# Performance work log

Measured on AMD Instinct MI355X. Metric: run time of the kernel, lower is better.

## Reference

```python
import jax, jax.numpy as jnp
import numpy as np

B, S, HID = 1, 2048, 2048
H, D = 16, 128          # num heads, head_dim (H*D == HID)
L = 32                  # compression / selection block size
NB = S // L             # number of key blocks
NSEL = 8                # top-n selected blocks per query
WIN = 512               # sliding window size
SCALE = 1.0 / np.sqrt(D)
NEG = -1e9


def rotate_half(x):
    x1, x2 = x[..., : x.shape[-1] // 2], x[..., x.shape[-1] // 2 :]
    return jnp.concatenate([-x2, x1], axis=-1)


def rope_tables(dim, end, theta=10000.0):
    freqs = 1.0 / theta ** (jnp.arange(0, dim, 2, dtype=jnp.float32) / dim)
    ang = jnp.outer(jnp.arange(end, dtype=jnp.float32), freqs)  # [end, dim/2]
    cos = jnp.concatenate([jnp.cos(ang), jnp.cos(ang)], axis=-1)  # [end, dim]
    sin = jnp.concatenate([jnp.sin(ang), jnp.sin(ang)], axis=-1)
    return cos, sin


def setup_inputs() -> dict:
    key = jax.random.key(0)
    ks = jax.random.split(key, 10)
    std = 0.02
    return {
        "hidden_states": jax.random.normal(ks[0], (B, S, HID), jnp.float32),
        "Wq": jax.random.normal(ks[1], (HID, H * D), jnp.float32) * std,
        "bq": jnp.zeros((H * D,), jnp.float32),
        "Wk": jax.random.normal(ks[2], (HID, H * D), jnp.float32) * std,
        "bk": jnp.zeros((H * D,), jnp.float32),
        "Wv": jax.random.normal(ks[3], (HID, H * D), jnp.float32) * std,
        "bv": jnp.zeros((H * D,), jnp.float32),
        "Wg": jax.random.normal(ks[4], (H, D, 3), jnp.float32) * std,
        "bg": jnp.zeros((3,), jnp.float32),
    }


def _nsa_forward(hidden_states, Wq, bq, Wk, bk, Wv, bv, Wg, bg):
    # projections -> [B, H, S, D]
    def proj(W, b):
        return (hidden_states @ W + b).reshape(B, S, H, D).transpose(0, 2, 1, 3)

    q, k, v = proj(Wq, bq), proj(Wk, bk), proj(Wv, bv)

    cos, sin = rope_tables(D, S)  # [S, D]
    cos, sin = cos[None, None], sin[None, None]
    q = q * cos + rotate_half(q) * sin
    k = k * cos + rotate_half(k) * sin

    i = jnp.arange(S)
    t = jnp.arange(S)
    causal = t[None, :] <= i[:, None]  # [S, S]

    # ---- compressed branch: block mean-pooled K/V ----
    k_cmp = k.reshape(B, H, NB, L, D).mean(axis=3)  # [B,H,NB,D]
    v_cmp = v.reshape(B, H, NB, L, D).mean(axis=3)
    # block j visible if it ends at or before query position i
    blk_ok = ((jnp.arange(NB) + 1) * L - 1)[None, :] <= i[:, None]  # [S, NB]
    s_cmp = jnp.einsum("bhid,bhjd->bhij", q, k_cmp) * SCALE  # [B,H,S,NB]
    p_cmp = jax.nn.softmax(jnp.where(blk_ok[None, None], s_cmp, NEG), axis=-1)
    has_blk = blk_ok.any(axis=-1).astype(q.dtype)[None, None, :, None]  # [1,1,S,1]
    out_cmp = jnp.einsum("bhij,bhjd->bhid", p_cmp, v_cmp) * has_blk

    # ---- selection branch: top-n blocks from compressed scores ----
    idx = jax.lax.top_k(p_cmp, NSEL)[1]  # [B,H,S,NSEL]
    block_sel = (idx[..., None] == jnp.arange(NB)).any(axis=-2)  # [B,H,S,NB]
    cur_blk = (i[:, None] // L) == jnp.arange(NB)[None, :]  # always include own block
    block_sel = block_sel | cur_blk[None, None]
    tok_sel = jnp.take(block_sel, t // L, axis=-1)  # [B,H,S,S]
    mask_sel = tok_sel & causal[None, None]

    s = jnp.einsum("bhid,bhjd->bhij", q, k) * SCALE
    p_sel = jax.nn.softmax(jnp.where(mask_sel, s, NEG), axis=-1)
    out_sel = jnp.einsum("bhij,bhjd->bhid", p_sel, v)

    # ---- sliding-window branch ----
    mask_win = causal & ((i[:, None] - t[None, :]) < WIN)
    p_win = jax.nn.softmax(jnp.where(mask_win[None, None], s, NEG), axis=-1)
    out_win = jnp.einsum("bhij,bhjd->bhid", p_win, v)

    # ---- gated combine ----
    g = jax.nn.sigmoid(jnp.einsum("bhsd,hdg->bhsg", q, Wg) + bg)  # [B,H,S,3]
    out = (g[..., 0:1] * out_cmp + g[..., 1:2] * out_sel + g[..., 2:3] * out_win)
    return out.transpose(0, 2, 1, 3).reshape(B, S, H * D)


def reference(hidden_states, Wq, bq, Wk, bk, Wv, bv, Wg, bg):
    return _nsa_forward(hidden_states, Wq, bq, Wk, bk, Wv, bv, Wg, bg)
```

## Files before the change

### kernel.cpp

```cpp
#include <hip/hip_runtime.h>


#define SCALE_F 0.08838834764831845f
#define SCL2E   (0.08838834764831845f * 1.4426950408889634f)

typedef short  bf16x8 __attribute__((ext_vector_type(8)));
typedef short  s16x4  __attribute__((ext_vector_type(4)));
typedef float  f32x4  __attribute__((ext_vector_type(4)));

__device__ __forceinline__ unsigned short f2bfu(float x){
    unsigned u = __builtin_bit_cast(unsigned, x);
    u = (u + 0x7FFFu + ((u >> 16) & 1u)) >> 16;
    return (unsigned short)u;
}
__device__ __forceinline__ float bf2f(unsigned short b){
    unsigned u = ((unsigned)b) << 16;
    return __builtin_bit_cast(float, u);
}
__device__ __forceinline__ f32x4 mfma16(bf16x8 a, bf16x8 b, f32x4 c){
    return __builtin_amdgcn_mfma_f32_16x16x32_bf16(a, b, c, 0, 0, 0);
}

__global__ __launch_bounds__(64) void rope_table_k(float* __restrict__ ct,
                                                   float* __restrict__ st){
    int s = blockIdx.x, j = threadIdx.x;
    float fr  = 1.0f / powf(10000.0f, (float)j * (1.0f / 64.0f));
    float ang = (float)s * fr;
    ct[s * 64 + j] = cosf(ang);
    st[s * 64 + j] = sinf(ang);
}

template <bool LO>
__global__ __launch_bounds__(256) void prep_split(const float* __restrict__ src,
                                                  unsigned short* __restrict__ hi,
                                                  unsigned short* __restrict__ lo){
    size_t i = ((size_t)blockIdx.x * 256 + threadIdx.x) * 4;
    float4 x = *(const float4*)&src[i];
    unsigned short h0 = f2bfu(x.x), h1 = f2bfu(x.y), h2 = f2bfu(x.z), h3 = f2bfu(x.w);
    s16x4 hv; hv[0] = (short)h0; hv[1] = (short)h1; hv[2] = (short)h2; hv[3] = (short)h3;
    *(s16x4*)&hi[i] = hv;
    if (LO){
        s16x4 lv;
        lv[0] = (short)f2bfu(x.x - bf2f(h0)); lv[1] = (short)f2bfu(x.y - bf2f(h1));
        lv[2] = (short)f2bfu(x.z - bf2f(h2)); lv[3] = (short)f2bfu(x.w - bf2f(h3));
        *(s16x4*)&lo[i] = lv;
    }
}

__global__ __launch_bounds__(256) void prep_wT(const float* __restrict__ W,
                                               unsigned short* __restrict__ Th,
                                               unsigned short* __restrict__ Tl){
    __shared__ float T[64][65];
    const int k0 = blockIdx.x * 64, n0 = blockIdx.y * 64;
    const int tid = (int)threadIdx.x;
    #pragma unroll
    for (int it = 0; it < 16; ++it){
        int idx = tid + it * 256;
        int r = idx >> 6, c = idx & 63;
        T[c][r] = W[(size_t)(k0 + r) * 2048 + n0 + c];
    }
    __syncthreads();
    #pragma unroll
    for (int it = 0; it < 16; ++it){
        int idx = tid + it * 256;
        int n = idx >> 6, k = idx & 63;
        float v = T[n][k];
        unsigned short h = f2bfu(v);
        Th[(size_t)(n0 + n) * 2048 + k0 + k] = h;
        if (Tl) Tl[(size_t)(n0 + n) * 2048 + k0 + k] = f2bfu(v - bf2f(h));
    }
}

template <int P>
__global__ __launch_bounds__(256) void gemm_bf(
    const unsigned short* __restrict__ Ah, const unsigned short* __restrict__ Al,
    const unsigned short* __restrict__ Bh, const unsigned short* __restrict__ Bl,
    const float* __restrict__ bias,
    float* __restrict__ outF, unsigned short* __restrict__ outT)
{
    const unsigned short* Ap[2] = {Ah, Al};
    const unsigned short* Bp[2] = {Bh, Bl};
    const int m0  = blockIdx.x * 128;
    const int h   = blockIdx.y;
    const int tid = (int)threadIdx.x;
    const int l   = tid & 63, w = tid >> 6;
    const int wr  = w >> 1,  wc = w & 1;
    const int cc  = l & 15,  g  = l >> 4;

    __shared__ short As[P][128][40];
    __shared__ short Bs[P][128][40];

    f32x4 acc[4][4] = {};
    bf16x8 ra[P][2], rb[P][2];

    auto LOADSTEP = [&](int k0){
        #pragma unroll
        for (int p = 0; p < P; ++p)
            #pragma unroll
            for (int it = 0; it < 2; ++it){
                int c = tid + it * 256;
                int row = c >> 2, col8 = (c & 3) * 8;
                ra[p][it] = *(const bf16x8*)&Ap[p][(size_t)(m0 + row) * 2048 + k0 + col8];
                rb[p][it] = *(const bf16x8*)&Bp[p][(size_t)(h * 128 + row) * 2048 + k0 + col8];
            }
    };
    auto STORESTEP = [&](){
        #pragma unroll
        for (int p = 0; p < P; ++p)
            #pragma unroll
            for (int it = 0; it < 2; ++it){
                int c = tid + it * 256;
                int row = c >> 2, col8 = (c & 3) * 8;
                *(bf16x8*)&As[p][row][col8] = ra[p][it];
                *(bf16x8*)&Bs[p][row][col8] = rb[p][it];
            }
    };

    LOADSTEP(0); STORESTEP(); __syncthreads();
    for (int k0 = 0; k0 < 2048; k0 += 32){
        bool more = (k0 + 32) < 2048;
        if (more) LOADSTEP(k0 + 32);

        bf16x8 ah[4], bh[4];
        #pragma unroll
        for (int mt = 0; mt < 4; ++mt)
            ah[mt] = *(const bf16x8*)&As[0][wr * 64 + mt * 16 + cc][g * 8];
        #pragma unroll
        for (int nt = 0; nt < 4; ++nt)
            bh[nt] = *(const bf16x8*)&Bs[0][wc * 64 + nt * 16 + cc][g * 8];
        if (P == 2){
            bf16x8 al[4], bl[4];
            #pragma unroll
            for (int mt = 0; mt < 4; ++mt)
                al[mt] = *(const bf16x8*)&As[P - 1][wr * 64 + mt * 16 + cc][g * 8];
            #pragma unroll
            for (int nt = 0; nt < 4; ++nt)
                bl[nt] = *(const bf16x8*)&Bs[P - 1][wc * 64 + nt * 16 + cc][g * 8];
            #pragma unroll
            for (int mt = 0; mt < 4; ++mt)
                #pragma unroll
                for (int nt = 0; nt < 4; ++nt){
                    acc[mt][nt] = mfma16(ah[mt], bh[nt], acc[mt][nt]);
                    acc[mt][nt] = mfma16(ah[mt], bl[nt], acc[mt][nt]);
                    acc[mt][nt] = mfma16(al[mt], bh[nt], acc[mt][nt]);
                }
        } else {
            #pragma unroll
            for (int mt = 0; mt < 4; ++mt)
                #pragma unroll
                for (int nt = 0; nt < 4; ++nt)
                    acc[mt][nt] = mfma16(ah[mt], bh[nt], acc[mt][nt]);
        }
        __syncthreads();
        if (more){ STORESTEP(); __syncthreads(); }
    }

    #pragma unroll
    for (int mt = 0; mt < 4; ++mt)
        #pragma unroll
        for (int nt = 0; nt < 4; ++nt)
            #pragma unroll
            for (int j = 0; j < 4; ++j){
                int srow = m0 + wr * 64 + mt * 16 + g * 4 + j;
                int col  = wc * 64 + nt * 16 + cc;
                float v = acc[mt][nt][j] + bias[h * 128 + col];
                if (outF) outF[((size_t)h * 2048 + srow) * 128 + col] = v;
                else      outT[((size_t)h * 128 + col) * 2048 + srow] = f2bfu(v);
            }
}

__global__ __launch_bounds__(256) void rope_apply(
    float* __restrict__ qf, float* __restrict__ kf,
    const float* __restrict__ ct, const float* __restrict__ st)
{
    int idx = blockIdx.x * 256 + (int)threadIdx.x;
    int j = idx & 63;
    int s = (idx >> 6) & 2047;
    int h = (idx >> 17) & 15;
    int a = idx >> 21;
    float* p = (a ? kf : qf) + ((size_t)h * 2048 + s) * 128;
    float c = ct[s * 64 + j], sn = st[s * 64 + j];
    float x1 = p[j], x2 = p[j + 64];
    p[j]      = x1 * c - x2 * sn;
    p[j + 64] = x2 * c + x1 * sn;
}

__global__ __launch_bounds__(256) void cmp_mean(
    const float* __restrict__ kf, const unsigned short* __restrict__ vtbf,
    float* __restrict__ kcmp, float* __restrict__ vcmp)
{
    int idx = blockIdx.x * 256 + (int)threadIdx.x;
    int d  = idx & 127;
    int nb = (idx >> 7) & 63;
    int h  = idx >> 13;
    const float* kp = &kf[((size_t)h * 2048 + nb * 32) * 128 + d];
    float sk = 0.f;
    #pragma unroll
    for (int t = 0; t < 32; ++t) sk += kp[t * 128];
    const unsigned short* vp = &vtbf[((size_t)h * 128 + d) * 2048 + nb * 32];
    float sv = 0.f;
    #pragma unroll
    for (int t = 0; t < 32; ++t) sv += bf2f(vp[t]);
    kcmp[((size_t)h * 64 + nb) * 128 + d] = sk * 0.03125f;
    vcmp[((size_t)h * 64 + nb) * 128 + d] = sv * 0.03125f;
}

__global__ __launch_bounds__(256) void gates_k(
    const float* __restrict__ qf, const float* __restrict__ Wg,
    const float* __restrict__ bg, float* __restrict__ gout)
{
    int Gn = blockIdx.x * 256 + (int)threadIdx.x;
    int sub = Gn & 3, qh = Gn >> 2;
    if (sub == 3) return;
    int h = qh >> 11;
    const float* q  = &qf[(size_t)qh * 128];
    const float* wg = &Wg[(size_t)h * 384 + sub];
    float acc = 0.f;
    #pragma unroll 4
    for (int k = 0; k < 128; ++k) acc += q[k] * wg[k * 3];
    gout[(size_t)qh * 3 + sub] = 1.f / (1.f + expf(-(acc + bg[sub])));
}

__global__ __launch_bounds__(256) void cmp_attn(
    const float* __restrict__ qf, const float* __restrict__ kcmp,
    const float* __restrict__ vcmp, const float* __restrict__ gout,
    float* __restrict__ out, unsigned long long* __restrict__ bmask)
{
    const int h = blockIdx.y, qt = blockIdx.x, i0 = qt * 64;
    const int tid = (int)threadIdx.x;
    const int l = tid & 63, w = tid >> 6;
    const int ty = tid >> 4, tx = tid & 15;
    const int cc = l & 15, g = l >> 4;

    __shared__ __align__(16) char smem[65536];
    float4* qs4 = (float4*)smem;
    float4* kc4 = (float4*)(smem + 32768);
    unsigned short* vcT = (unsigned short*)smem;
    float* sc = (float*)(smem + 32768);
    unsigned short* ps = (unsigned short*)(smem + 32768 + 17408);

    #pragma unroll
    for (int it = 0; it < 8; ++it){
        int idx = tid + it * 256;
        int row = idx >> 5, c = idx & 31;
        int cs = c ^ ((row >> 2) & 7);
        qs4[row * 32 + cs] = *(const float4*)&qf[((size_t)h * 2048 + i0 + row) * 128 + c * 4];
        kc4[row * 32 + cs] = *(const float4*)&kcmp[((size_t)h * 64 + row) * 128 + c * 4];
    }
    __syncthreads();

    float acc[4][4] = {};
    #pragma unroll 2
    for (int k0 = 0; k0 < 32; ++k0){
        float4 qv[4], kv[4];
        #pragma unroll
        for (int j = 0; j < 4; ++j) qv[j] = qs4[(4 * ty + j) * 32 + (k0 ^ (ty & 7))];
        #pragma unroll
        for (int c = 0; c < 4; ++c) kv[c] = kc4[(4 * tx + c) * 32 + (k0 ^ (tx & 7))];
        #pragma unroll
        for (int j = 0; j < 4; ++j)
            #pragma unroll
            for (int c = 0; c < 4; ++c)
                acc[j][c] += qv[j].x * kv[c].x + qv[j].y * kv[c].y
                           + qv[j].z * kv[c].z + qv[j].w * kv[c].w;
    }
    __syncthreads();

    #pragma unroll
    for (int j = 0; j < 4; ++j){
        int r = 4 * ty + j, i = i0 + r;
        float4 sv;
        float* svp = (float*)&sv;
        #pragma unroll
        for (int c = 0; c < 4; ++c){
            int b = 4 * tx + c;
            svp[c] = (b * 32 + 31 <= i) ? acc[j][c] * SCALE_F : -1e9f;
        }
        *(float4*)&sc[r * 68 + 4 * tx] = sv;
    }
    #pragma unroll
    for (int it = 0; it < 8; ++it){
        int idx = tid + it * 256;
        int jb = idx >> 5, d4 = (idx & 31) * 4;
        float4 vx = *(const float4*)&vcmp[((size_t)h * 64 + jb) * 128 + d4];
        const float* vp = (const float*)&vx;
        #pragma unroll
        for (int jj = 0; jj < 4; ++jj)
            vcT[(d4 + jj) * 72 + jb] = f2bfu(vp[jj]);
    }
    __syncthreads();

    for (int qq = 0; qq < 16; ++qq){
        const int q = w * 16 + qq;
        float s = sc[q * 68 + l];
        float mx = s;
        #pragma unroll
        for (int off = 1; off < 64; off <<= 1) mx = fmaxf(mx, __shfl_xor(mx, off));
        float p = expf(s - mx);
        float sum = p;
        #pragma unroll
        for (int off = 1; off < 64; off <<= 1) sum += __shfl_xor(sum, off);
        p /= sum;
        ps[q * 72 + l] = f2bfu(p);

        unsigned long long sel = 1ULL << ((i0 + q) >> 5);
        unsigned long long key = (1ULL << 45) |
            ((unsigned long long)__builtin_bit_cast(unsigned, p) << 7) |
            (unsigned long long)(63 - l);
        #pragma unroll
        for (int it = 0; it < 8; ++it){
            unsigned long long k2 = key;
            #pragma unroll
            for (int off = 1; off < 64; off <<= 1){
                unsigned long long o = __shfl_xor(k2, off);
                k2 = (o > k2) ? o : k2;
            }
            int wb = 63 - (int)(k2 & 63ULL);
            sel |= 1ULL << wb;
            if (l == wb) key = 0ULL;
        }
        if (l == 0) bmask[(size_t)h * 2048 + i0 + q] = sel;
    }
    __syncthreads();

    f32x4 oacc[8] = {};
    #pragma unroll
    for (int kk = 0; kk < 2; ++kk){
        bf16x8 pa = *(const bf16x8*)&ps[(w * 16 + cc) * 72 + kk * 32 + g * 8];
        #pragma unroll
        for (int nt2 = 0; nt2 < 8; ++nt2){
            bf16x8 vfr = *(const bf16x8*)&vcT[(nt2 * 16 + cc) * 72 + kk * 32 + g * 8];
            oacc[nt2] = mfma16(pa, vfr, oacc[nt2]);
        }
    }
    #pragma unroll
    for (int j = 0; j < 4; ++j){
        int q = w * 16 + g * 4 + j, iq = i0 + q;
        float g0 = gout[((size_t)h * 2048 + iq) * 3];
        float f = (iq >= 31) ? g0 : 0.f;
        #pragma unroll
        for (int nt2 = 0; nt2 < 8; ++nt2)
            out[(size_t)iq * 2048 + h * 128 + nt2 * 16 + cc] = f * oacc[nt2][j];
    }
}

template <bool IS_SEL>
__global__ __launch_bounds__(256) void attn_main(
    const unsigned short* __restrict__ qbf,
    const unsigned short* __restrict__ kbf,
    const unsigned short* __restrict__ vtbf,
    const float* __restrict__ gates,
    const unsigned long long* __restrict__ bmask,
    float* __restrict__ out)
{
    const int h  = blockIdx.y;
    const int qt = IS_SEL ? 31 - (int)blockIdx.x : (int)blockIdx.x;
    const int i0 = qt * 64;
    const int tid = (int)threadIdx.x;
    const int l = tid & 63, w = tid >> 6;
    const int cc = l & 15,  g = l >> 4;

    __shared__ short Ks[64][136];
    __shared__ short Vt[128][72];
    __shared__ short Ps[4][16][72];

    unsigned long long um = 0;
    if (IS_SEL){
        um = bmask[(size_t)h * 2048 + i0 + l];
        #pragma unroll
        for (int off = 1; off < 64; off <<= 1) um |= __shfl_xor(um, off);
    }

    unsigned long long bm[4];
    int mrow[4];
    #pragma unroll
    for (int j = 0; j < 4; ++j){
        mrow[j] = i0 + w * 16 + g * 4 + j;
        bm[j] = IS_SEL ? bmask[(size_t)h * 2048 + mrow[j]] : 0ULL;
    }

    bf16x8 qfrag[4];
    {
        const unsigned short* qrow = &qbf[((size_t)h * 2048 + i0 + w * 16 + cc) * 128];
        #pragma unroll
        for (int kk = 0; kk < 4; ++kk)
            qfrag[kk] = *(const bf16x8*)&qrow[kk * 32 + g * 8];
    }

    f32x4 oacc[8] = {};
    float mrun[4], lrun[4];
    #pragma unroll
    for (int j = 0; j < 4; ++j){ mrun[j] = -1e30f; lrun[j] = 0.f; }

    const int chlo = IS_SEL ? 0 : (qt > 8 ? qt - 8 : 0);
    auto needed = [&](int ch)->bool {
        return IS_SEL ? (((um >> (2 * ch)) & 3ULL) != 0ULL) : true;
    };

    bf16x8 rk[4], rv[4];
    auto LOADC = [&](int ch){
        #pragma unroll
        for (int it = 0; it < 4; ++it){
            int c = tid + it * 256;
            rk[it] = *(const bf16x8*)&kbf[((size_t)h * 2048 + ch * 64 + (c >> 4)) * 128 + (c & 15) * 8];
            rv[it] = *(const bf16x8*)&vtbf[((size_t)h * 128 + (c >> 3)) * 2048 + ch * 64 + (c & 7) * 8];
        }
    };
    auto STOREC = [&](){
        #pragma unroll
        for (int it = 0; it < 4; ++it){
            int c = tid + it * 256;
            *(bf16x8*)&Ks[c >> 4][(c & 15) * 8] = rk[it];
            *(bf16x8*)&Vt[c >> 3][(c & 7) * 8] = rv[it];
        }
    };

    int cur = chlo;
    while (cur <= qt && !needed(cur)) ++cur;
    LOADC(cur); STOREC(); __syncthreads();

    while (cur <= qt){
        int nxt = cur + 1;
        while (nxt <= qt && !needed(nxt)) ++nxt;
        const bool more = (nxt <= qt);
        if (more) LOADC(nxt);

        f32x4 sacc[4] = {};
        #pragma unroll
        for (int kk = 0; kk < 4; ++kk)
            #pragma unroll
            for (int nt = 0; nt < 4; ++nt){
                bf16x8 kfr = *(const bf16x8*)&Ks[nt * 16 + cc][kk * 32 + g * 8];
                sacc[nt] = mfma16(qfrag[kk], kfr, sacc[nt]);
            }

        const int tbase = cur * 64;
        #pragma unroll
        for (int j = 0; j < 4; ++j){
            const int iq = mrow[j];
            float sj[4]; bool ok[4];
            float mx = -1e30f;
            #pragma unroll
            for (int nt = 0; nt < 4; ++nt){
                int t = tbase + nt * 16 + cc;
                bool o = (t <= iq) &&
                         (IS_SEL ? (((bm[j] >> (t >> 5)) & 1ULL) != 0ULL)
                                 : ((iq - t) < 512));
                float s = sacc[nt][j] * SCL2E;
                sj[nt] = s; ok[nt] = o;
                if (o) mx = fmaxf(mx, s);
            }
            #pragma unroll
            for (int off = 1; off < 16; off <<= 1)
                mx = fmaxf(mx, __shfl_xor(mx, off));
            float mnew = fmaxf(mrun[j], mx);
            float alpha = exp2f(mrun[j] - mnew);
            float psum = 0.f;
            #pragma unroll
            for (int nt = 0; nt < 4; ++nt){
                float p = ok[nt] ? exp2f(sj[nt] - mnew) : 0.f;
                psum += p;
                Ps[w][g * 4 + j][nt * 16 + cc] = (short)f2bfu(p);
            }
            #pragma unroll
            for (int off = 1; off < 16; off <<= 1)
                psum += __shfl_xor(psum, off);
            mrun[j] = mnew;
            lrun[j] = lrun[j] * alpha + psum;
            #pragma unroll
            for (int nt2 = 0; nt2 < 8; ++nt2) oacc[nt2][j] *= alpha;
        }
        __syncthreads();

        #pragma unroll
        for (int kk = 0; kk < 2; ++kk){
            bf16x8 pa = *(const bf16x8*)&Ps[w][cc][kk * 32 + g * 8];
            #pragma unroll
            for (int nt2 = 0; nt2 < 8; ++nt2){
                bf16x8 vfr = *(const bf16x8*)&Vt[nt2 * 16 + cc][kk * 32 + g * 8];
                oacc[nt2] = mfma16(pa, vfr, oacc[nt2]);
            }
        }
        __syncthreads();
        if (more){ STOREC(); __syncthreads(); }
        cur = more ? nxt : qt + 1;
    }

    const int GI = IS_SEL ? 1 : 2;
    #pragma unroll
    for (int j = 0; j < 4; ++j){
        const int iq = mrow[j];
        float gv  = gates[((size_t)h * 2048 + iq) * 3 + GI];
        float inv = gv / lrun[j];
        #pragma unroll
        for (int nt2 = 0; nt2 < 8; ++nt2){
            int d = nt2 * 16 + cc;
            out[(size_t)iq * 2048 + h * 128 + d] += oacc[nt2][j] * inv;
        }
    }
}

#define MB ((size_t)1 << 20)
#define OFF_QF   ((size_t)0)
#define OFF_KF   (16 * MB)
#define OFF_VT   (32 * MB)
#define OFF_XH   (40 * MB)
#define OFF_XL   (48 * MB)
#define OFF_WTH  (56 * MB)
#define OFF_WTL  (64 * MB)
#define OFF_COS  (72 * MB)
#define OFF_SIN  (72 * MB + 524288)
#define OFF_KC   (72 * MB + 1048576)
#define OFF_VC   (72 * MB + 1572864)
#define OFF_GATE (72 * MB + 2097152)
#define OFF_BM   (72 * MB + 2490368)

extern "C" void kernel_launch(void* const* d_in, const int* in_sizes, int n_in,
                              void* d_out, int out_size, void* d_ws, size_t ws_size,
                              hipStream_t stream)
{
    const float* X  = (const float*)d_in[0];
    const float* Wq = (const float*)d_in[1];
    const float* bq = (const float*)d_in[2];
    const float* Wk = (const float*)d_in[3];
    const float* bk = (const float*)d_in[4];
    const float* Wv = (const float*)d_in[5];
    const float* bv = (const float*)d_in[6];
    const float* Wg = (const float*)d_in[7];
    const float* bg = (const float*)d_in[8];
    float* out = (float*)d_out;

    char* ws = (char*)d_ws;
    float* qf   = (float*)(ws + OFF_QF);
    float* kf   = (float*)(ws + OFF_KF);
    unsigned short* vtbf = (unsigned short*)(ws + OFF_VT);
    unsigned short* Xh   = (unsigned short*)(ws + OFF_XH);
    unsigned short* Xl   = (unsigned short*)(ws + OFF_XL);
    unsigned short* WTh  = (unsigned short*)(ws + OFF_WTH);
    unsigned short* WTl  = (unsigned short*)(ws + OFF_WTL);
    unsigned short* qbf  = (unsigned short*)(ws + OFF_XH);
    unsigned short* kbf  = (unsigned short*)(ws + OFF_XL);
    float* cost  = (float*)(ws + OFF_COS);
    float* sint  = (float*)(ws + OFF_SIN);
    float* kcmp  = (float*)(ws + OFF_KC);
    float* vcmp  = (float*)(ws + OFF_VC);
    float* gatesb = (float*)(ws + OFF_GATE);
    unsigned long long* bmaskb = (unsigned long long*)(ws + OFF_BM);

    rope_table_k<<<2048, 64, 0, stream>>>(cost, sint);
    prep_split<true><<<4096, 256, 0, stream>>>(X, Xh, Xl);

    prep_wT<<<dim3(32, 32), 256, 0, stream>>>(Wq, WTh, WTl);
    gemm_bf<2><<<dim3(16, 16), 256, 0, stream>>>(Xh, Xl, WTh, WTl, bq, qf, nullptr);
    prep_wT<<<dim3(32, 32), 256, 0, stream>>>(Wk, WTh, WTl);
    gemm_bf<2><<<dim3(16, 16), 256, 0, stream>>>(Xh, Xl, WTh, WTl, bk, kf, nullptr);
    prep_wT<<<dim3(32, 32), 256, 0, stream>>>(Wv, WTh, nullptr);
    gemm_bf<1><<<dim3(16, 16), 256, 0, stream>>>(Xh, nullptr, WTh, nullptr, bv, nullptr, vtbf);

    rope_apply<<<16384, 256, 0, stream>>>(qf, kf, cost, sint);
    prep_split<false><<<4096, 256, 0, stream>>>(qf, qbf, nullptr);
    prep_split<false><<<4096, 256, 0, stream>>>(kf, kbf, nullptr);

    cmp_mean<<<512, 256, 0, stream>>>(kf, vtbf, kcmp, vcmp);
    gates_k<<<512, 256, 0, stream>>>(qf, Wg, bg, gatesb);
    cmp_attn<<<dim3(32, 16), 256, 0, stream>>>(qf, kcmp, vcmp, gatesb, out, bmaskb);

    attn_main<false><<<dim3(32, 16), 256, 0, stream>>>(qbf, kbf, vtbf, gatesb, bmaskb, out);
    attn_main<true><<<dim3(32, 16), 256, 0, stream>>>(qbf, kbf, vtbf, gatesb, bmaskb, out);
}
```

Measured before the change: 597.7 us.

## Batch QKV projections, fuse gates and bf16 conversion, merge attention branches

Merges the three weight transposes and three projection GEMMs into single z-indexed launches when the workspace is large enough. RoPE now writes bf16 copies directly, so two conversion passes are dropped. The gate computation moves into the compressed-attention kernel. The selected and sliding-window attention kernels become one launch with atomic output accumulation, XOR-swizzled shared memory and a lazy-rescale online softmax. These changes cut launch count, memory passes and bank conflicts. In exchange they add atomics, a workspace-size dependence and the possibility of a different floating-point summation order.

```diff
diff --git a/kernel.cpp b/kernel.cpp
--- a/kernel.cpp
+++ b/kernel.cpp
@@ -30,7 +30,6 @@
     st[s * 64 + j] = sinf(ang);
 }
 
-template <bool LO>
 __global__ __launch_bounds__(256) void prep_split(const float* __restrict__ src,
                                                   unsigned short* __restrict__ hi,
                                                   unsigned short* __restrict__ lo){
@@ -39,17 +38,24 @@
     unsigned short h0 = f2bfu(x.x), h1 = f2bfu(x.y), h2 = f2bfu(x.z), h3 = f2bfu(x.w);
     s16x4 hv; hv[0] = (short)h0; hv[1] = (short)h1; hv[2] = (short)h2; hv[3] = (short)h3;
     *(s16x4*)&hi[i] = hv;
-    if (LO){
-        s16x4 lv;
-        lv[0] = (short)f2bfu(x.x - bf2f(h0)); lv[1] = (short)f2bfu(x.y - bf2f(h1));
-        lv[2] = (short)f2bfu(x.z - bf2f(h2)); lv[3] = (short)f2bfu(x.w - bf2f(h3));
-        *(s16x4*)&lo[i] = lv;
-    }
-}
-
-__global__ __launch_bounds__(256) void prep_wT(const float* __restrict__ W,
-                                               unsigned short* __restrict__ Th,
-                                               unsigned short* __restrict__ Tl){
+    s16x4 lv;
+    lv[0] = (short)f2bfu(x.x - bf2f(h0)); lv[1] = (short)f2bfu(x.y - bf2f(h1));
+    lv[2] = (short)f2bfu(x.z - bf2f(h2)); lv[3] = (short)f2bfu(x.w - bf2f(h3));
+    *(s16x4*)&lo[i] = lv;
+}
+
+__global__ __launch_bounds__(256) void prep_wT3(
+    const float* __restrict__ W0, const float* __restrict__ W1,
+    const float* __restrict__ W2,
+    unsigned short* __restrict__ Th0, unsigned short* __restrict__ Tl0,
+    unsigned short* __restrict__ Th1, unsigned short* __restrict__ Tl1,
+    unsigned short* __restrict__ Th2)
+{
+    const int z = blockIdx.z;
+    const float* W = (z == 0) ? W0 : (z == 1) ? W1 : W2;
+    unsigned short* Th = (z == 0) ? Th0 : (z == 1) ? Th1 : Th2;
+    unsigned short* Tl = (z == 0) ? Tl0 : (z == 1) ? Tl1 : nullptr;
+
     __shared__ float T[64][65];
     const int k0 = blockIdx.x * 64, n0 = blockIdx.y * 64;
     const int tid = (int)threadIdx.x;
@@ -71,15 +77,22 @@
     }
 }
 
-template <int P>
-__global__ __launch_bounds__(256) void gemm_bf(
-    const unsigned short* __restrict__ Ah, const unsigned short* __restrict__ Al,
-    const unsigned short* __restrict__ Bh, const unsigned short* __restrict__ Bl,
-    const float* __restrict__ bias,
-    float* __restrict__ outF, unsigned short* __restrict__ outT)
+__global__ __launch_bounds__(256, 3) void gemm3(
+    const unsigned short* __restrict__ Xh, const unsigned short* __restrict__ Xl,
+    const unsigned short* __restrict__ Bqh, const unsigned short* __restrict__ Bql,
+    const unsigned short* __restrict__ Bkh, const unsigned short* __restrict__ Bkl,
+    const unsigned short* __restrict__ Bvh,
+    const float* __restrict__ bq, const float* __restrict__ bk,
+    const float* __restrict__ bv,
+    float* __restrict__ qf, float* __restrict__ kf,
+    unsigned short* __restrict__ vtbf, int zbase)
 {
-    const unsigned short* Ap[2] = {Ah, Al};
-    const unsigned short* Bp[2] = {Bh, Bl};
+    const int z = zbase + (int)blockIdx.z;
+    const bool split = (z < 2);
+    const unsigned short* Bh = (z == 0) ? Bqh : (z == 1) ? Bkh : Bvh;
+    const unsigned short* Bl = (z == 0) ? Bql : Bkl;
+    const float* bias        = (z == 0) ? bq  : (z == 1) ? bk  : bv;
+
     const int m0  = blockIdx.x * 128;
     const int h   = blockIdx.y;
     const int tid = (int)threadIdx.x;
@@ -87,33 +100,37 @@
     const int wr  = w >> 1,  wc = w & 1;
     const int cc  = l & 15,  g  = l >> 4;
 
-    __shared__ short As[P][128][40];
-    __shared__ short Bs[P][128][40];
+    __shared__ short As[2][128][40];
+    __shared__ short Bs[2][128][40];
 
     f32x4 acc[4][4] = {};
-    bf16x8 ra[P][2], rb[P][2];
+    bf16x8 rah[2], ral[2], rbh[2], rbl[2];
 
     auto LOADSTEP = [&](int k0){
         #pragma unroll
-        for (int p = 0; p < P; ++p)
-            #pragma unroll
-            for (int it = 0; it < 2; ++it){
-                int c = tid + it * 256;
-                int row = c >> 2, col8 = (c & 3) * 8;
-                ra[p][it] = *(const bf16x8*)&Ap[p][(size_t)(m0 + row) * 2048 + k0 + col8];
-                rb[p][it] = *(const bf16x8*)&Bp[p][(size_t)(h * 128 + row) * 2048 + k0 + col8];
-            }
+        for (int it = 0; it < 2; ++it){
+            int c = tid + it * 256;
+            int row = c >> 2, col8 = (c & 3) * 8;
+            rah[it] = *(const bf16x8*)&Xh[(size_t)(m0 + row) * 2048 + k0 + col8];
+            rbh[it] = *(const bf16x8*)&Bh[(size_t)(h * 128 + row) * 2048 + k0 + col8];
+            if (split){
+                ral[it] = *(const bf16x8*)&Xl[(size_t)(m0 + row) * 2048 + k0 + col8];
+                rbl[it] = *(const bf16x8*)&Bl[(size_t)(h * 128 + row) * 2048 + k0 + col8];
+            }
+        }
     };
     auto STORESTEP = [&](){
         #pragma unroll
-        for (int p = 0; p < P; ++p)
-            #pragma unroll
-            for (int it = 0; it < 2; ++it){
-                int c = tid + it * 256;
-                int row = c >> 2, col8 = (c & 3) * 8;
-                *(bf16x8*)&As[p][row][col8] = ra[p][it];
-                *(bf16x8*)&Bs[p][row][col8] = rb[p][it];
-            }
+        for (int it = 0; it < 2; ++it){
+            int c = tid + it * 256;
+            int row = c >> 2, col8 = (c & 3) * 8;
+            *(bf16x8*)&As[0][row][col8] = rah[it];
+            *(bf16x8*)&Bs[0][row][col8] = rbh[it];
+            if (split){
+                *(bf16x8*)&As[1][row][col8] = ral[it];
+                *(bf16x8*)&Bs[1][row][col8] = rbl[it];
+            }
+        }
     };
 
     LOADSTEP(0); STORESTEP(); __syncthreads();
@@ -128,14 +145,14 @@
         #pragma unroll
         for (int nt = 0; nt < 4; ++nt)
             bh[nt] = *(const bf16x8*)&Bs[0][wc * 64 + nt * 16 + cc][g * 8];
-        if (P == 2){
+        if (split){
             bf16x8 al[4], bl[4];
             #pragma unroll
             for (int mt = 0; mt < 4; ++mt)
-                al[mt] = *(const bf16x8*)&As[P - 1][wr * 64 + mt * 16 + cc][g * 8];
+                al[mt] = *(const bf16x8*)&As[1][wr * 64 + mt * 16 + cc][g * 8];
             #pragma unroll
             for (int nt = 0; nt < 4; ++nt)
-                bl[nt] = *(const bf16x8*)&Bs[P - 1][wc * 64 + nt * 16 + cc][g * 8];
+                bl[nt] = *(const bf16x8*)&Bs[1][wc * 64 + nt * 16 + cc][g * 8];
             #pragma unroll
             for (int mt = 0; mt < 4; ++mt)
                 #pragma unroll
@@ -164,13 +181,15 @@
                 int srow = m0 + wr * 64 + mt * 16 + g * 4 + j;
                 int col  = wc * 64 + nt * 16 + cc;
                 float v = acc[mt][nt][j] + bias[h * 128 + col];
-                if (outF) outF[((size_t)h * 2048 + srow) * 128 + col] = v;
-                else      outT[((size_t)h * 128 + col) * 2048 + srow] = f2bfu(v);
+                if (z == 0)      qf[((size_t)h * 2048 + srow) * 128 + col] = v;
+                else if (z == 1) kf[((size_t)h * 2048 + srow) * 128 + col] = v;
+                else             vtbf[((size_t)h * 128 + col) * 2048 + srow] = f2bfu(v);
             }
 }
 
 __global__ __launch_bounds__(256) void rope_apply(
     float* __restrict__ qf, float* __restrict__ kf,
+    unsigned short* __restrict__ qbb, unsigned short* __restrict__ kbb,
     const float* __restrict__ ct, const float* __restrict__ st)
 {
     int idx = blockIdx.x * 256 + (int)threadIdx.x;
@@ -178,11 +197,15 @@
     int s = (idx >> 6) & 2047;
     int h = (idx >> 17) & 15;
     int a = idx >> 21;
-    float* p = (a ? kf : qf) + ((size_t)h * 2048 + s) * 128;
+    size_t off = ((size_t)h * 2048 + s) * 128;
+    float* p = (a ? kf : qf) + off;
+    unsigned short* pb = (a ? kbb : qbb) + off;
     float c = ct[s * 64 + j], sn = st[s * 64 + j];
     float x1 = p[j], x2 = p[j + 64];
-    p[j]      = x1 * c - x2 * sn;
-    p[j + 64] = x2 * c + x1 * sn;
+    float y1 = x1 * c - x2 * sn;
+    float y2 = x2 * c + x1 * sn;
+    p[j]      = y1;  p[j + 64]  = y2;
+    pb[j] = f2bfu(y1); pb[j + 64] = f2bfu(y2);
 }
 
 __global__ __launch_bounds__(256) void cmp_mean(
@@ -205,26 +228,12 @@
     vcmp[((size_t)h * 64 + nb) * 128 + d] = sv * 0.03125f;
 }
 
-__global__ __launch_bounds__(256) void gates_k(
-    const float* __restrict__ qf, const float* __restrict__ Wg,
-    const float* __restrict__ bg, float* __restrict__ gout)
-{
-    int Gn = blockIdx.x * 256 + (int)threadIdx.x;
-    int sub = Gn & 3, qh = Gn >> 2;
-    if (sub == 3) return;
-    int h = qh >> 11;
-    const float* q  = &qf[(size_t)qh * 128];
-    const float* wg = &Wg[(size_t)h * 384 + sub];
-    float acc = 0.f;
-    #pragma unroll 4
-    for (int k = 0; k < 128; ++k) acc += q[k] * wg[k * 3];
-    gout[(size_t)qh * 3 + sub] = 1.f / (1.f + expf(-(acc + bg[sub])));
-}
-
 __global__ __launch_bounds__(256) void cmp_attn(
     const float* __restrict__ qf, const float* __restrict__ kcmp,
-    const float* __restrict__ vcmp, const float* __restrict__ gout,
-    float* __restrict__ out, unsigned long long* __restrict__ bmask)
+    const float* __restrict__ vcmp,
+    const float* __restrict__ Wg, const float* __restrict__ bg,
+    float* __restrict__ out, float* __restrict__ gout,
+    unsigned long long* __restrict__ bmask)
 {
     const int h = blockIdx.y, qt = blockIdx.x, i0 = qt * 64;
     const int tid = (int)threadIdx.x;
@@ -233,6 +242,7 @@
     const int cc = l & 15, g = l >> 4;
 
     __shared__ __align__(16) char smem[65536];
+    __shared__ float sgl[4][16][3];
     float4* qs4 = (float4*)smem;
     float4* kc4 = (float4*)(smem + 32768);
     unsigned short* vcT = (unsigned short*)smem;
@@ -249,6 +259,23 @@
     }
     __syncthreads();
 
+    {
+        int gi = l & 3, qq = l >> 2;
+        if (gi < 3){
+            int q = w * 16 + qq;
+            float acc = 0.f;
+            #pragma unroll
+            for (int c = 0; c < 32; ++c){
+                float4 qv = qs4[q * 32 + (c ^ ((q >> 2) & 7))];
+                const float* wgp = &Wg[(size_t)h * 384 + (c * 4) * 3 + gi];
+                acc += qv.x * wgp[0] + qv.y * wgp[3] + qv.z * wgp[6] + qv.w * wgp[9];
+            }
+            float gv = 1.f / (1.f + expf(-(acc + bg[gi])));
+            sgl[w][qq][gi] = gv;
+            gout[((size_t)h * 2048 + i0 + q) * 3 + gi] = gv;
+        }
+    }
+
     float acc[4][4] = {};
     #pragma unroll 2
     for (int k0 = 0; k0 < 32; ++k0){
@@ -336,7 +363,7 @@
     #pragma unroll
     for (int j = 0; j < 4; ++j){
         int q = w * 16 + g * 4 + j, iq = i0 + q;
-        float g0 = gout[((size_t)h * 2048 + iq) * 3];
+        float g0 = sgl[w][g * 4 + j][0];
         float f = (iq >= 31) ? g0 : 0.f;
         #pragma unroll
         for (int nt2 = 0; nt2 < 8; ++nt2)
@@ -344,8 +371,7 @@
     }
 }
 
-template <bool IS_SEL>
-__global__ __launch_bounds__(256) void attn_main(
+__global__ __launch_bounds__(256, 3) void attn_ws(
     const unsigned short* __restrict__ qbf,
     const unsigned short* __restrict__ kbf,
     const unsigned short* __restrict__ vtbf,
@@ -354,18 +380,19 @@
     float* __restrict__ out)
 {
     const int h  = blockIdx.y;
-    const int qt = IS_SEL ? 31 - (int)blockIdx.x : (int)blockIdx.x;
+    const bool SEL = ((int)blockIdx.x < 32);
+    const int qt = SEL ? 31 - (int)blockIdx.x : 63 - (int)blockIdx.x;
     const int i0 = qt * 64;
     const int tid = (int)threadIdx.x;
     const int l = tid & 63, w = tid >> 6;
     const int cc = l & 15,  g = l >> 4;
 
-    __shared__ short Ks[64][136];
-    __shared__ short Vt[128][72];
-    __shared__ short Ps[4][16][72];
+    __shared__ short Ks[64 * 128];
+    __shared__ short Vt[128 * 64];
+    __shared__ short Ps[4][16 * 64];
 
     unsigned long long um = 0;
-    if (IS_SEL){
+    if (SEL){
         um = bmask[(size_t)h * 2048 + i0 + l];
         #pragma unroll
         for (int off = 1; off < 64; off <<= 1) um |= __shfl_xor(um, off);
@@ -376,7 +403,7 @@
     #pragma unroll
     for (int j = 0; j < 4; ++j){
         mrow[j] = i0 + w * 16 + g * 4 + j;
-        bm[j] = IS_SEL ? bmask[(size_t)h * 2048 + mrow[j]] : 0ULL;
+        bm[j] = SEL ? bmask[(size_t)h * 2048 + mrow[j]] : 0ULL;
     }
 
     bf16x8 qfrag[4];
@@ -388,13 +415,13 @@
     }
 
     f32x4 oacc[8] = {};
-    float mrun[4], lrun[4];
-    #pragma unroll
-    for (int j = 0; j < 4; ++j){ mrun[j] = -1e30f; lrun[j] = 0.f; }
-
-    const int chlo = IS_SEL ? 0 : (qt > 8 ? qt - 8 : 0);
+    float mrun[4], lsum[4];
+    #pragma unroll
+    for (int j = 0; j < 4; ++j){ mrun[j] = -1e30f; lsum[j] = 0.f; }
+
+    const int chlo = SEL ? 0 : (qt > 8 ? qt - 8 : 0);
     auto needed = [&](int ch)->bool {
-        return IS_SEL ? (((um >> (2 * ch)) & 3ULL) != 0ULL) : true;
+        return SEL ? (((um >> (2 * ch)) & 3ULL) != 0ULL) : true;
     };
 
     bf16x8 rk[4], rv[4];
@@ -402,16 +429,20 @@
         #pragma unroll
         for (int it = 0; it < 4; ++it){
             int c = tid + it * 256;
-            rk[it] = *(const bf16x8*)&kbf[((size_t)h * 2048 + ch * 64 + (c >> 4)) * 128 + (c & 15) * 8];
-            rv[it] = *(const bf16x8*)&vtbf[((size_t)h * 128 + (c >> 3)) * 2048 + ch * 64 + (c & 7) * 8];
+            int tok = c >> 4, d8 = c & 15;
+            rk[it] = *(const bf16x8*)&kbf[((size_t)h * 2048 + ch * 64 + tok) * 128 + d8 * 8];
+            int vd = c >> 3, t8 = c & 7;
+            rv[it] = *(const bf16x8*)&vtbf[((size_t)h * 128 + vd) * 2048 + ch * 64 + t8 * 8];
         }
     };
     auto STOREC = [&](){
         #pragma unroll
         for (int it = 0; it < 4; ++it){
             int c = tid + it * 256;
-            *(bf16x8*)&Ks[c >> 4][(c & 15) * 8] = rk[it];
-            *(bf16x8*)&Vt[c >> 3][(c & 7) * 8] = rv[it];
+            int tok = c >> 4, d8 = c & 15;
+            *(bf16x8*)&Ks[tok * 128 + ((d8 ^ (tok & 7)) << 3)] = rk[it];
+            int vd = c >> 3, t8 = c & 7;
+            *(bf16x8*)&Vt[vd * 64 + ((t8 ^ (vd & 7)) << 3)] = rv[it];
         }
     };
 
@@ -430,7 +461,8 @@
         for (int kk = 0; kk < 4; ++kk)
             #pragma unroll
             for (int nt = 0; nt < 4; ++nt){
-                bf16x8 kfr = *(const bf16x8*)&Ks[nt * 16 + cc][kk * 32 + g * 8];
+                bf16x8 kfr = *(const bf16x8*)
+                    &Ks[(nt * 16 + cc) * 128 + (((kk * 4 + g) ^ (cc & 7)) << 3)];
                 sacc[nt] = mfma16(qfrag[kk], kfr, sacc[nt]);
             }
 
@@ -438,14 +470,15 @@
         #pragma unroll
         for (int j = 0; j < 4; ++j){
             const int iq = mrow[j];
+            const int row = g * 4 + j;
             float sj[4]; bool ok[4];
             float mx = -1e30f;
             #pragma unroll
             for (int nt = 0; nt < 4; ++nt){
                 int t = tbase + nt * 16 + cc;
                 bool o = (t <= iq) &&
-                         (IS_SEL ? (((bm[j] >> (t >> 5)) & 1ULL) != 0ULL)
-                                 : ((iq - t) < 512));
+                         (SEL ? (((bm[j] >> (t >> 5)) & 1ULL) != 0ULL)
+                              : ((iq - t) < 512));
                 float s = sacc[nt][j] * SCL2E;
                 sj[nt] = s; ok[nt] = o;
                 if (o) mx = fmaxf(mx, s);
@@ -453,31 +486,33 @@
             #pragma unroll
             for (int off = 1; off < 16; off <<= 1)
                 mx = fmaxf(mx, __shfl_xor(mx, off));
-            float mnew = fmaxf(mrun[j], mx);
-            float alpha = exp2f(mrun[j] - mnew);
-            float psum = 0.f;
+            float mo = mrun[j];
+            if (mx > mo + 8.f){
+                float al = exp2f(mo - mx);
+                mrun[j] = mo = mx;
+                lsum[j] *= al;
+                #pragma unroll
+                for (int nt2 = 0; nt2 < 8; ++nt2) oacc[nt2][j] *= al;
+            }
+            float pacc = 0.f;
             #pragma unroll
             for (int nt = 0; nt < 4; ++nt){
-                float p = ok[nt] ? exp2f(sj[nt] - mnew) : 0.f;
-                psum += p;
-                Ps[w][g * 4 + j][nt * 16 + cc] = (short)f2bfu(p);
-            }
-            #pragma unroll
-            for (int off = 1; off < 16; off <<= 1)
-                psum += __shfl_xor(psum, off);
-            mrun[j] = mnew;
-            lrun[j] = lrun[j] * alpha + psum;
-            #pragma unroll
-            for (int nt2 = 0; nt2 < 8; ++nt2) oacc[nt2][j] *= alpha;
-        }
-        __syncthreads();
+                float p = ok[nt] ? exp2f(sj[nt] - mo) : 0.f;
+                pacc += p;
+                Ps[w][row * 64 + ((nt * 16 + cc) ^ ((row & 7) << 3))] = (short)f2bfu(p);
+            }
+            lsum[j] += pacc;
+        }
 
         #pragma unroll
         for (int kk = 0; kk < 2; ++kk){
-            bf16x8 pa = *(const bf16x8*)&Ps[w][cc][kk * 32 + g * 8];
+            bf16x8 pa = *(const bf16x8*)
+                &Ps[w][cc * 64 + (((kk * 4 + g) ^ (cc & 7)) << 3)];
             #pragma unroll
             for (int nt2 = 0; nt2 < 8; ++nt2){
-                bf16x8 vfr = *(const bf16x8*)&Vt[nt2 * 16 + cc][kk * 32 + g * 8];
+                int vd = nt2 * 16 + cc;
+                bf16x8 vfr = *(const bf16x8*)
+                    &Vt[vd * 64 + (((kk * 4 + g) ^ (cc & 7)) << 3)];
                 oacc[nt2] = mfma16(pa, vfr, oacc[nt2]);
             }
         }
@@ -486,34 +521,22 @@
         cur = more ? nxt : qt + 1;
     }
 
-    const int GI = IS_SEL ? 1 : 2;
+    const int GI = SEL ? 1 : 2;
     #pragma unroll
     for (int j = 0; j < 4; ++j){
+        float ls = lsum[j];
+        #pragma unroll
+        for (int off = 1; off < 16; off <<= 1) ls += __shfl_xor(ls, off);
         const int iq = mrow[j];
         float gv  = gates[((size_t)h * 2048 + iq) * 3 + GI];
-        float inv = gv / lrun[j];
+        float inv = gv / ls;
         #pragma unroll
         for (int nt2 = 0; nt2 < 8; ++nt2){
             int d = nt2 * 16 + cc;
-            out[(size_t)iq * 2048 + h * 128 + d] += oacc[nt2][j] * inv;
-        }
-    }
-}
-
-#define MB ((size_t)1 << 20)
-#define OFF_QF   ((size_t)0)
-#define OFF_KF   (16 * MB)
-#define OFF_VT   (32 * MB)
-#define OFF_XH   (40 * MB)
-#define OFF_XL   (48 * MB)
-#define OFF_WTH  (56 * MB)
-#define OFF_WTL  (64 * MB)
-#define OFF_COS  (72 * MB)
-#define OFF_SIN  (72 * MB + 524288)
-#define OFF_KC   (72 * MB + 1048576)
-#define OFF_VC   (72 * MB + 1572864)
-#define OFF_GATE (72 * MB + 2097152)
-#define OFF_BM   (72 * MB + 2490368)
+            atomicAdd(&out[(size_t)iq * 2048 + h * 128 + d], oacc[nt2][j] * inv);
+        }
+    }
+}
 
 extern "C" void kernel_launch(void* const* d_in, const int* in_sizes, int n_in,
                               void* d_out, int out_size, void* d_ws, size_t ws_size,
@@ -530,41 +553,72 @@
     const float* bg = (const float*)d_in[8];
     float* out = (float*)d_out;
 
+    const size_t MBs = (size_t)1 << 20;
     char* ws = (char*)d_ws;
-    float* qf   = (float*)(ws + OFF_QF);
-    float* kf   = (float*)(ws + OFF_KF);
-    unsigned short* vtbf = (unsigned short*)(ws + OFF_VT);
-    unsigned short* Xh   = (unsigned short*)(ws + OFF_XH);
-    unsigned short* Xl   = (unsigned short*)(ws + OFF_XL);
-    unsigned short* WTh  = (unsigned short*)(ws + OFF_WTH);
-    unsigned short* WTl  = (unsigned short*)(ws + OFF_WTL);
-    unsigned short* qbf  = (unsigned short*)(ws + OFF_XH);
-    unsigned short* kbf  = (unsigned short*)(ws + OFF_XL);
-    float* cost  = (float*)(ws + OFF_COS);
-    float* sint  = (float*)(ws + OFF_SIN);
-    float* kcmp  = (float*)(ws + OFF_KC);
-    float* vcmp  = (float*)(ws + OFF_VC);
-    float* gatesb = (float*)(ws + OFF_GATE);
-    unsigned long long* bmaskb = (unsigned long long*)(ws + OFF_BM);
+    const bool bigws = ws_size >= 100 * MBs;
+
+    unsigned short *Xh, *Xl, *WQH, *WQL, *WKH, *WKL, *WVH;
+    float *qf, *kf;
+    unsigned short *vtbf, *qbf, *kbf;
+    size_t SM;
+    if (bigws){
+        Xh  = (unsigned short*)(ws + 0 * MBs);
+        Xl  = (unsigned short*)(ws + 8 * MBs);
+        WQH = (unsigned short*)(ws + 16 * MBs);
+        WQL = (unsigned short*)(ws + 24 * MBs);
+        WKH = (unsigned short*)(ws + 32 * MBs);
+        WKL = (unsigned short*)(ws + 40 * MBs);
+        WVH = (unsigned short*)(ws + 48 * MBs);
+        qf  = (float*)(ws + 56 * MBs);
+        kf  = (float*)(ws + 72 * MBs);
+        vtbf = (unsigned short*)(ws + 88 * MBs);
+        qbf = WQH; kbf = WQL;
+        SM  = 96 * MBs;
+    } else {
+        Xh  = (unsigned short*)(ws + 0 * MBs);
+        Xl  = (unsigned short*)(ws + 8 * MBs);
+        WQH = WKH = WVH = (unsigned short*)(ws + 16 * MBs);
+        WQL = WKL       = (unsigned short*)(ws + 24 * MBs);
+        qf  = (float*)(ws + 32 * MBs);
+        kf  = (float*)(ws + 48 * MBs);
+        vtbf = (unsigned short*)(ws + 64 * MBs);
+        qbf = (unsigned short*)(ws + 16 * MBs);
+        kbf = (unsigned short*)(ws + 24 * MBs);
+        SM  = 72 * MBs;
+    }
+    float* cost  = (float*)(ws + SM);
+    float* sint  = (float*)(ws + SM + 524288);
+    float* kcmp  = (float*)(ws + SM + 1048576);
+    float* vcmp  = (float*)(ws + SM + 1572864);
+    float* gatesb = (float*)(ws + SM + 2097152);
+    unsigned long long* bmaskb = (unsigned long long*)(ws + SM + 2097152 + 393216);
 
     rope_table_k<<<2048, 64, 0, stream>>>(cost, sint);
-    prep_split<true><<<4096, 256, 0, stream>>>(X, Xh, Xl);
-
-    prep_wT<<<dim3(32, 32), 256, 0, stream>>>(Wq, WTh, WTl);
-    gemm_bf<2><<<dim3(16, 16), 256, 0, stream>>>(Xh, Xl, WTh, WTl, bq, qf, nullptr);
-    prep_wT<<<dim3(32, 32), 256, 0, stream>>>(Wk, WTh, WTl);
-    gemm_bf<2><<<dim3(16, 16), 256, 0, stream>>>(Xh, Xl, WTh, WTl, bk, kf, nullptr);
-    prep_wT<<<dim3(32, 32), 256, 0, stream>>>(Wv, WTh, nullptr);
-    gemm_bf<1><<<dim3(16, 16), 256, 0, stream>>>(Xh, nullptr, WTh, nullptr, bv, nullptr, vtbf);
-
-    rope_apply<<<16384, 256, 0, stream>>>(qf, kf, cost, sint);
-    prep_split<false><<<4096, 256, 0, stream>>>(qf, qbf, nullptr);
-    prep_split<false><<<4096, 256, 0, stream>>>(kf, kbf, nullptr);
-
+    prep_split<<<4096, 256, 0, stream>>>(X, Xh, Xl);
+
+    if (bigws){
+        prep_wT3<<<dim3(32, 32, 3), 256, 0, stream>>>(Wq, Wk, Wv,
+                                                      WQH, WQL, WKH, WKL, WVH);
+        gemm3<<<dim3(16, 16, 3), 256, 0, stream>>>(Xh, Xl, WQH, WQL, WKH, WKL,
+                                                   WVH, bq, bk, bv, qf, kf, vtbf, 0);
+    } else {
+        prep_wT3<<<dim3(32, 32, 1), 256, 0, stream>>>(Wq, nullptr, nullptr,
+                                                      WQH, WQL, nullptr, nullptr, nullptr);
+        gemm3<<<dim3(16, 16, 1), 256, 0, stream>>>(Xh, Xl, WQH, WQL, WKH, WKL,
+                                                   WVH, bq, bk, bv, qf, kf, vtbf, 0);
+        prep_wT3<<<dim3(32, 32, 1), 256, 0, stream>>>(Wk, nullptr, nullptr,
+                                                      WKH, WKL, nullptr, nullptr, nullptr);
+        gemm3<<<dim3(16, 16, 1), 256, 0, stream>>>(Xh, Xl, WQH, WQL, WKH, WKL,
+                                                   WVH, bq, bk, bv, qf, kf, vtbf, 1);
+        prep_wT3<<<dim3(32, 32, 1), 256, 0, stream>>>(Wv, nullptr, nullptr,
+                                                      WVH, nullptr, nullptr, nullptr, nullptr);
+        gemm3<<<dim3(16, 16, 1), 256, 0, stream>>>(Xh, Xl, WQH, WQL, WKH, WKL,
+                                                   WVH, bq, bk, bv, qf, kf, vtbf, 2);
+    }
+
+    rope_apply<<<16384, 256, 0, stream>>>(qf, kf, qbf, kbf, cost, sint);
     cmp_mean<<<512, 256, 0, stream>>>(kf, vtbf, kcmp, vcmp);
-    gates_k<<<512, 256, 0, stream>>>(qf, Wg, bg, gatesb);
-    cmp_attn<<<dim3(32, 16), 256, 0, stream>>>(qf, kcmp, vcmp, gatesb, out, bmaskb);
-
-    attn_main<false><<<dim3(32, 16), 256, 0, stream>>>(qbf, kbf, vtbf, gatesb, bmaskb, out);
-    attn_main<true><<<dim3(32, 16), 256, 0, stream>>>(qbf, kbf, vtbf, gatesb, bmaskb, out);
-}
+    cmp_attn<<<dim3(32, 16), 256, 0, stream>>>(qf, kcmp, vcmp, Wg, bg,
+                                               out, gatesb, bmaskb);
+    attn_ws<<<dim3(64, 16), 256, 0, stream>>>(qbf, kbf, vtbf, gatesb, bmaskb, out);
+}
```

Measured after the change: 1.291 ms. 2.16x slower.
